# Kernel tuning notes

Measured on AMD Instinct MI355X. Metric: run time of the kernel, lower is better.

## Reference

```python
import jax, jax.numpy as jnp
import numpy as np

B, T, C, H = 8, 2048, 1024, 128

def setup_inputs() -> dict:
    key = jax.random.key(0)
    k1, k2, k3, k4 = jax.random.split(key, 4)
    s = 1.0 / np.sqrt(C)
    return {
        "x": jax.random.normal(k1, (B, T, C), dtype=jnp.float32),
        "Wq": jax.random.normal(k2, (C, H), dtype=jnp.float32) * s,
        "Wk": jax.random.normal(k3, (C, H), dtype=jnp.float32) * s,
        "Wv": jax.random.normal(k4, (C, H), dtype=jnp.float32) * s,
    }

def reference(x, Wq, Wk, Wv):
    # q,k,v: [B,T,H]
    q = jnp.einsum('btc,ch->bth', x, Wq)
    k = jnp.einsum('btc,ch->bth', x, Wk)
    v = jnp.einsum('btc,ch->bth', x, Wv)
    scale = k.shape[-1] ** -0.5
    wei = jnp.einsum('bqh,bkh->bqk', q, k) * scale  # [B,T,T]
    # NOTE: original forward never applies the tril mask -> full bidirectional softmax
    wei = jax.nn.softmax(wei, axis=-1)
    # dropout p=0 (eval): identity
    out = jnp.einsum('bqk,bkh->bqh', wei, v)  # [B,T,H]
    return out
```

## Files before the change

kernel.cpp:

```cpp
#include <hip/hip_runtime.h>

typedef __attribute__((ext_vector_type(4))) float  f32x4;
typedef __attribute__((ext_vector_type(8))) short  s16x8;
typedef __attribute__((ext_vector_type(4))) unsigned int u32x4;
typedef __attribute__((ext_vector_type(4))) unsigned short u16x4;

#define NB 8
#define NT 2048
#define NC 1024
#define NH 128
#define NM (NB * NT)

__device__ __forceinline__ unsigned short f2bf(float f) {
  union { float f; unsigned u; } v; v.f = f;
  unsigned r = v.u + 0x7FFFu + ((v.u >> 16) & 1u);
  return (unsigned short)(r >> 16);
}
__device__ __forceinline__ unsigned pack2(float a, float b) {
  return (unsigned)f2bf(a) | ((unsigned)f2bf(b) << 16);
}
__device__ __forceinline__ f32x4 mfma16(s16x8 a, s16x8 b, f32x4 c) {
  return __builtin_amdgcn_mfma_f32_16x16x32_bf16(a, b, c, 0, 0, 0);
}

__global__ __launch_bounds__(256) void k_prep_w(
    const float* __restrict__ wq, const float* __restrict__ wk,
    const float* __restrict__ wv, unsigned short* __restrict__ wt3) {
  __shared__ float ts[64][65];
  const int tid = threadIdx.x;
  const int w = blockIdx.x >> 5;
  const int rem = blockIdx.x & 31;
  const int c0 = (rem >> 1) * 64;
  const int h0 = (rem & 1) * 64;
  const float* W = (w == 0) ? wq : (w == 1) ? wk : wv;
  const int hl = tid & 63, ci = tid >> 6;
  #pragma unroll
  for (int i = 0; i < 16; ++i) {
    int cl = i * 4 + ci;
    ts[cl][hl] = W[(size_t)(c0 + cl) * NH + h0 + hl];
  }
  __syncthreads();
  const int cl2 = tid & 63, hi2 = tid >> 6;
  #pragma unroll
  for (int j = 0; j < 16; ++j) {
    int hl2 = j * 4 + hi2;
    float v = ts[cl2][hl2];
    if (w == 0) v *= 0.08838834764831845f;
    wt3[(size_t)w * 131072 + (size_t)(h0 + hl2) * NC + c0 + cl2] = f2bf(v);
  }
}

__global__ __launch_bounds__(512) void k_qkv(
    const float* __restrict__ x, const unsigned short* __restrict__ wt3,
    unsigned short* __restrict__ qo, unsigned short* __restrict__ ko,
    unsigned short* __restrict__ vo) {
  __shared__ u32x4 xs4[2 * 64 * 128 / 16];
  char* xs = (char*)xs4;
  const int tid = threadIdx.x;
  const int lane = tid & 63;
  const int w = tid >> 6;
  const int m0 = blockIdx.x * 64;

  const int sr = tid >> 3;
  const float* xp = x + (size_t)(m0 + sr) * NC + (tid & 7) * 8;
  const int wb = (sr * 128 + (tid & 7) * 16) ^ ((sr & 7) << 4);

  const int mg = w >> 2;
  const int n0 = (w & 3) * 96;
  const int arow0 = mg * 32 + (lane & 15);
  const int aswz = (arow0 & 7) << 4;
  const int akb = (lane >> 4) * 16;

  f32x4 acc[2][6] = {};
  f32x4 xa = *(const f32x4*)(xp);
  f32x4 xb = *(const f32x4*)(xp + 4);
  {
    u32x4 pk = { pack2(xa.x, xa.y), pack2(xa.z, xa.w),
                 pack2(xb.x, xb.y), pack2(xb.z, xb.w) };
    *(u32x4*)(xs + wb) = pk;
  }
  __syncthreads();

  for (int kt = 0; kt < 16; ++kt) {
    if (kt < 15) {
      xa = *(const f32x4*)(xp + (kt + 1) * 64);
      xb = *(const f32x4*)(xp + (kt + 1) * 64 + 4);
    }
    char* cb = xs + (kt & 1) * 8192;
    #pragma unroll
    for (int ks = 0; ks < 2; ++ks) {
      s16x8 a0 = *(const s16x8*)(cb + (((arow0)      * 128 + ks * 64 + akb) ^ aswz));
      s16x8 a1 = *(const s16x8*)(cb + (((arow0 + 16) * 128 + ks * 64 + akb) ^ aswz));
      const unsigned short* wp = wt3 + (size_t)(n0 + (lane & 15)) * NC
                                 + kt * 64 + ks * 32 + (lane >> 4) * 8;
      #pragma unroll
      for (int nj = 0; nj < 6; ++nj) {
        s16x8 bf = *(const s16x8*)(wp + (size_t)nj * 16 * NC);
        acc[0][nj] = mfma16(a0, bf, acc[0][nj]);
        acc[1][nj] = mfma16(a1, bf, acc[1][nj]);
      }
    }
    if (kt < 15) {
      u32x4 pk = { pack2(xa.x, xa.y), pack2(xa.z, xa.w),
                   pack2(xb.x, xb.y), pack2(xb.z, xb.w) };
      *(u32x4*)(xs + ((kt + 1) & 1) * 8192 + wb) = pk;
    }
    __syncthreads();
  }
  const int rl = (lane >> 4) * 4;
  #pragma unroll
  for (int m = 0; m < 2; ++m) {
    #pragma unroll
    for (int nj = 0; nj < 6; ++nj) {
      f32x4 a = acc[m][nj];
      int gcol = n0 + nj * 16 + (lane & 15);
      int gr = m0 + mg * 32 + m * 16 + rl;
      int h = gcol & 127;
      if (gcol < 256) {
        unsigned short* dst = (gcol < 128) ? qo : ko;
        dst[(size_t)(gr + 0) * NH + h] = f2bf(a.x);
        dst[(size_t)(gr + 1) * NH + h] = f2bf(a.y);
        dst[(size_t)(gr + 2) * NH + h] = f2bf(a.z);
        dst[(size_t)(gr + 3) * NH + h] = f2bf(a.w);
      } else {
        int bb = gr >> 11, tt = gr & 2047;
        u16x4 pv = { f2bf(a.x), f2bf(a.y), f2bf(a.z), f2bf(a.w) };
        *(u16x4*)(vo + ((size_t)(bb * NH + h) * NT + tt)) = pv;
      }
    }
  }
}

__global__ __launch_bounds__(512) void k_attn(
    const unsigned short* __restrict__ qg, const unsigned short* __restrict__ kg,
    const unsigned short* __restrict__ vg, float* __restrict__ out) {
  __shared__ u32x4 lds4[147456 / 16];
  char* L = (char*)lds4;
  const int tid = threadIdx.x;
  const int lane = tid & 63;
  const int w = tid >> 6;
  const int grp = w >> 2;
  const int wq = w & 3;
  const int gt = tid & 255;
  const int b = blockIdx.y;
  const int qr = blockIdx.x * 64 + wq * 16;
  const int c15 = lane & 15;
  const int g4 = lane >> 4;
  const int kv0 = grp * 1024;

  char* Kb0 = L + grp * 65536;
  char* Vb0 = L + grp * 65536 + 32768;
  char* pw  = L + 131072 + w * 2048;

  s16x8 qf[4];
  #pragma unroll
  for (int ks = 0; ks < 4; ++ks)
    qf[ks] = *(const s16x8*)(qg + (size_t)(b * NT + qr + c15) * NH + ks * 32 + g4 * 8);

  float m_run[4], lsum[4];
  #pragma unroll
  for (int r = 0; r < 4; ++r) { m_run[r] = -3.0e38f; lsum[r] = 0.0f; }
  f32x4 acc_o[8] = {};

  const int skr = gt >> 4;
  const unsigned short* kbase = kg + (size_t)(b * NT + kv0) * NH + (gt & 15) * 8;
  const int svh = gt >> 3;
  const unsigned short* vbase = vg + (size_t)(b * NH) * NT + kv0 + (gt & 7) * 8;

  u32x4 kreg[4], vreg[4];
  #pragma unroll
  for (int i = 0; i < 4; ++i) {
    kreg[i] = *(const u32x4*)(kbase + (size_t)(skr + i * 16) * NH);
    vreg[i] = *(const u32x4*)(vbase + (size_t)(svh + i * 32) * NT);
  }
  auto write_tiles = [&](char* Kd, char* Vd) {
    #pragma unroll
    for (int i = 0; i < 4; ++i) {
      int r = skr + i * 16;
      *(u32x4*)(Kd + ((r * 256 + (gt & 15) * 16) ^ ((r & 7) << 4))) = kreg[i];
      int h = svh + i * 32;
      *(u32x4*)(Vd + ((h * 128 + (gt & 7) * 16) ^ ((h & 7) << 4))) = vreg[i];
    }
  };
  write_tiles(Kb0, Vb0);
  __syncthreads();

  for (int kt = 0; kt < 16; ++kt) {
    char* Ks = Kb0 + (kt & 1) * 16384;
    char* Vs = Vb0 + (kt & 1) * 16384;
    if (kt < 15) {
      #pragma unroll
      for (int i = 0; i < 4; ++i) {
        kreg[i] = *(const u32x4*)(kbase + (size_t)((kt + 1) * 64 + skr + i * 16) * NH);
        vreg[i] = *(const u32x4*)(vbase + (size_t)(svh + i * 32) * NT + (kt + 1) * 64);
      }
    }
    f32x4 s[4] = {};
    __builtin_amdgcn_s_setprio(1);
    #pragma unroll
    for (int nj = 0; nj < 4; ++nj) {
      int krow = nj * 16 + c15;
      int kswz = (krow & 7) << 4;
      #pragma unroll
      for (int ks = 0; ks < 4; ++ks) {
        s16x8 bf = *(const s16x8*)(Ks + ((krow * 256 + ks * 64 + g4 * 16) ^ kswz));
        s[nj] = mfma16(qf[ks], bf, s[nj]);
      }
    }
    __builtin_amdgcn_s_setprio(0);
    float alpha[4];
    #pragma unroll
    for (int r = 0; r < 4; ++r) {
      float pm = fmaxf(fmaxf(s[0][r], s[1][r]), fmaxf(s[2][r], s[3][r]));
      pm = fmaxf(pm, __shfl_xor(pm, 1));
      pm = fmaxf(pm, __shfl_xor(pm, 2));
      pm = fmaxf(pm, __shfl_xor(pm, 4));
      pm = fmaxf(pm, __shfl_xor(pm, 8));
      float mn = fmaxf(m_run[r], pm);
      alpha[r] = __expf(m_run[r] - mn);
      m_run[r] = mn;
      float e0 = __expf(s[0][r] - mn);
      float e1 = __expf(s[1][r] - mn);
      float e2 = __expf(s[2][r] - mn);
      float e3 = __expf(s[3][r] - mn);
      s[0][r] = e0; s[1][r] = e1; s[2][r] = e2; s[3][r] = e3;
      lsum[r] = lsum[r] * alpha[r] + (e0 + e1 + e2 + e3);
    }
    #pragma unroll
    for (int hj = 0; hj < 8; ++hj) {
      acc_o[hj][0] *= alpha[0]; acc_o[hj][1] *= alpha[1];
      acc_o[hj][2] *= alpha[2]; acc_o[hj][3] *= alpha[3];
    }
    #pragma unroll
    for (int nj = 0; nj < 4; ++nj) {
      int colb = (nj * 16 + c15) * 2;
      #pragma unroll
      for (int r = 0; r < 4; ++r) {
        int row = g4 * 4 + r;
        *(unsigned short*)(pw + ((row * 128 + colb) ^ ((row & 7) << 4))) = f2bf(s[nj][r]);
      }
    }
    __builtin_amdgcn_s_setprio(1);
    #pragma unroll
    for (int ks2 = 0; ks2 < 2; ++ks2) {
      s16x8 pa = *(const s16x8*)(pw + ((c15 * 128 + ks2 * 64 + g4 * 16) ^ ((c15 & 7) << 4)));
      #pragma unroll
      for (int hj = 0; hj < 8; ++hj) {
        int vrow = hj * 16 + c15;
        s16x8 bv = *(const s16x8*)(Vs + ((vrow * 128 + ks2 * 64 + g4 * 16) ^ ((vrow & 7) << 4)));
        acc_o[hj] = mfma16(pa, bv, acc_o[hj]);
      }
    }
    __builtin_amdgcn_s_setprio(0);
    if (kt < 15) write_tiles(Kb0 + ((kt + 1) & 1) * 16384, Vb0 + ((kt + 1) & 1) * 16384);
    __syncthreads();
  }
  float l_run[4];
  #pragma unroll
  for (int r = 0; r < 4; ++r) {
    float ls = lsum[r];
    ls += __shfl_xor(ls, 1);
    ls += __shfl_xor(ls, 2);
    ls += __shfl_xor(ls, 4);
    ls += __shfl_xor(ls, 8);
    l_run[r] = ls;
  }
  float* msh = (float*)(L + 32768);
  float* lsh = (float*)(L + 32768 + 256);
  if (grp == 1) {
    #pragma unroll
    for (int r = 0; r < 4; ++r) {
      int row = wq * 16 + g4 * 4 + r;
      #pragma unroll
      for (int hj = 0; hj < 8; ++hj)
        *(float*)(L + ((row * 512 + (hj * 16 + c15) * 4) ^ ((row & 7) << 4))) = acc_o[hj][r];
      if (c15 == 0) { msh[row] = m_run[r]; lsh[row] = l_run[r]; }
    }
  }
  __syncthreads();
  if (grp == 0) {
    #pragma unroll
    for (int r = 0; r < 4; ++r) {
      int row = wq * 16 + g4 * 4 + r;
      float m1 = msh[row], l1 = lsh[row];
      float M = fmaxf(m_run[r], m1);
      float w0 = __expf(m_run[r] - M);
      float w1 = __expf(m1 - M);
      float den = 1.0f / (w0 * l_run[r] + w1 * l1);
      #pragma unroll
      for (int hj = 0; hj < 8; ++hj) {
        float o1 = *(const float*)(L + ((row * 512 + (hj * 16 + c15) * 4) ^ ((row & 7) << 4)));
        out[(size_t)(b * NT + qr + g4 * 4 + r) * NH + hj * 16 + c15] =
            (w0 * acc_o[hj][r] + w1 * o1) * den;
      }
    }
  }
}

extern "C" void kernel_launch(void* const* d_in, const int* in_sizes, int n_in,
                              void* d_out, int out_size, void* d_ws, size_t ws_size,
                              hipStream_t stream) {
  const float* x  = (const float*)d_in[0];
  const float* wq = (const float*)d_in[1];
  const float* wk = (const float*)d_in[2];
  const float* wv = (const float*)d_in[3];
  unsigned short* ws  = (unsigned short*)d_ws;
  unsigned short* qb  = ws;
  unsigned short* kb  = ws + (size_t)2 * 1024 * 1024;
  unsigned short* vb  = ws + (size_t)4 * 1024 * 1024;
  unsigned short* wt3 = ws + (size_t)6 * 1024 * 1024;

  k_prep_w<<<dim3(96), dim3(256), 0, stream>>>(wq, wk, wv, wt3);
  k_qkv<<<dim3(NM / 64), dim3(512), 0, stream>>>(x, wt3, qb, kb, vb);
  k_attn<<<dim3(NT / 64, NB), dim3(512), 0, stream>>>(qb, kb, vb, (float*)d_out);
}
```

Measured before the change: 189.3 us.

## Shrink tiles and split attention KV across four wave groups for occupancy

The QKV projection now uses 32-row blocks with each wave covering 48 output columns, which doubles the grid and shrinks LDS. The attention kernel now splits KV four ways, with 512 keys per group. It processes 32 query rows per block using 32-key tiles held in a single LDS buffer, so LDS drops from about 144KB to about 73KB. Four partial softmax states are merged at the end. The aim is more resident blocks per CU and better latency hiding, but the loss of double buffering adds an extra barrier per iteration, and the MFMA work per sync is smaller.

```diff
diff --git a/kernel.cpp b/kernel.cpp
--- a/kernel.cpp
+++ b/kernel.cpp
@@ -3,6 +3,7 @@
 typedef __attribute__((ext_vector_type(4))) float  f32x4;
 typedef __attribute__((ext_vector_type(8))) short  s16x8;
 typedef __attribute__((ext_vector_type(4))) unsigned int u32x4;
+typedef __attribute__((ext_vector_type(2))) unsigned int u32x2;
 typedef __attribute__((ext_vector_type(4))) unsigned short u16x4;
 
 #define NB 8
@@ -50,71 +51,65 @@
   }
 }
 
-__global__ __launch_bounds__(512) void k_qkv(
+__global__ __launch_bounds__(512, 4) void k_qkv(
     const float* __restrict__ x, const unsigned short* __restrict__ wt3,
     unsigned short* __restrict__ qo, unsigned short* __restrict__ ko,
     unsigned short* __restrict__ vo) {
-  __shared__ u32x4 xs4[2 * 64 * 128 / 16];
+  __shared__ u32x4 xs4[8192 / 16];
   char* xs = (char*)xs4;
   const int tid = threadIdx.x;
   const int lane = tid & 63;
   const int w = tid >> 6;
-  const int m0 = blockIdx.x * 64;
-
-  const int sr = tid >> 3;
-  const float* xp = x + (size_t)(m0 + sr) * NC + (tid & 7) * 8;
-  const int wb = (sr * 128 + (tid & 7) * 16) ^ ((sr & 7) << 4);
-
-  const int mg = w >> 2;
-  const int n0 = (w & 3) * 96;
-  const int arow0 = mg * 32 + (lane & 15);
-  const int aswz = (arow0 & 7) << 4;
-  const int akb = (lane >> 4) * 16;
-
-  f32x4 acc[2][6] = {};
-  f32x4 xa = *(const f32x4*)(xp);
-  f32x4 xb = *(const f32x4*)(xp + 4);
+  const int m0 = blockIdx.x * 32;
+  const int c15 = lane & 15;
+  const int g4 = lane >> 4;
+
+  const int sr = tid >> 4;
+  const float* xp = x + (size_t)(m0 + sr) * NC + (tid & 15) * 4;
+  const int wb = (sr * 128 + (tid & 15) * 8) ^ ((sr & 7) << 4);
+
+  const int n0 = w * 48;
+  const int aswz = (c15 & 7) << 4;
+  const int akb = g4 * 16;
+
+  f32x4 acc[2][3] = {};
+  f32x4 xr = *(const f32x4*)(xp);
   {
-    u32x4 pk = { pack2(xa.x, xa.y), pack2(xa.z, xa.w),
-                 pack2(xb.x, xb.y), pack2(xb.z, xb.w) };
-    *(u32x4*)(xs + wb) = pk;
+    u32x2 pk = { pack2(xr.x, xr.y), pack2(xr.z, xr.w) };
+    *(u32x2*)(xs + wb) = pk;
   }
   __syncthreads();
 
   for (int kt = 0; kt < 16; ++kt) {
-    if (kt < 15) {
-      xa = *(const f32x4*)(xp + (kt + 1) * 64);
-      xb = *(const f32x4*)(xp + (kt + 1) * 64 + 4);
-    }
-    char* cb = xs + (kt & 1) * 8192;
+    if (kt < 15) xr = *(const f32x4*)(xp + (kt + 1) * 64);
+    char* cb = xs + (kt & 1) * 4096;
     #pragma unroll
     for (int ks = 0; ks < 2; ++ks) {
-      s16x8 a0 = *(const s16x8*)(cb + (((arow0)      * 128 + ks * 64 + akb) ^ aswz));
-      s16x8 a1 = *(const s16x8*)(cb + (((arow0 + 16) * 128 + ks * 64 + akb) ^ aswz));
-      const unsigned short* wp = wt3 + (size_t)(n0 + (lane & 15)) * NC
-                                 + kt * 64 + ks * 32 + (lane >> 4) * 8;
-      #pragma unroll
-      for (int nj = 0; nj < 6; ++nj) {
+      s16x8 a0 = *(const s16x8*)(cb + (((c15)      * 128 + ks * 64 + akb) ^ aswz));
+      s16x8 a1 = *(const s16x8*)(cb + (((c15 + 16) * 128 + ks * 64 + akb) ^ aswz));
+      const unsigned short* wp = wt3 + (size_t)(n0 + c15) * NC
+                                 + kt * 64 + ks * 32 + g4 * 8;
+      #pragma unroll
+      for (int nj = 0; nj < 3; ++nj) {
         s16x8 bf = *(const s16x8*)(wp + (size_t)nj * 16 * NC);
         acc[0][nj] = mfma16(a0, bf, acc[0][nj]);
         acc[1][nj] = mfma16(a1, bf, acc[1][nj]);
       }
     }
     if (kt < 15) {
-      u32x4 pk = { pack2(xa.x, xa.y), pack2(xa.z, xa.w),
-                   pack2(xb.x, xb.y), pack2(xb.z, xb.w) };
-      *(u32x4*)(xs + ((kt + 1) & 1) * 8192 + wb) = pk;
+      u32x2 pk = { pack2(xr.x, xr.y), pack2(xr.z, xr.w) };
+      *(u32x2*)(xs + ((kt + 1) & 1) * 4096 + wb) = pk;
     }
     __syncthreads();
   }
-  const int rl = (lane >> 4) * 4;
+  const int rl = g4 * 4;
   #pragma unroll
   for (int m = 0; m < 2; ++m) {
     #pragma unroll
-    for (int nj = 0; nj < 6; ++nj) {
+    for (int nj = 0; nj < 3; ++nj) {
       f32x4 a = acc[m][nj];
-      int gcol = n0 + nj * 16 + (lane & 15);
-      int gr = m0 + mg * 32 + m * 16 + rl;
+      int gcol = n0 + nj * 16 + c15;
+      int gr = m0 + m * 16 + rl;
       int h = gcol & 127;
       if (gcol < 256) {
         unsigned short* dst = (gcol < 128) ? qo : ko;
@@ -131,79 +126,79 @@
   }
 }
 
-__global__ __launch_bounds__(512) void k_attn(
+__global__ __launch_bounds__(512, 4) void k_attn(
     const unsigned short* __restrict__ qg, const unsigned short* __restrict__ kg,
     const unsigned short* __restrict__ vg, float* __restrict__ out) {
-  __shared__ u32x4 lds4[147456 / 16];
+  __shared__ u32x4 lds4[74752 / 16];
   char* L = (char*)lds4;
   const int tid = threadIdx.x;
   const int lane = tid & 63;
   const int w = tid >> 6;
-  const int grp = w >> 2;
-  const int wq = w & 3;
-  const int gt = tid & 255;
+  const int grp = w & 3;
+  const int qs = w >> 2;
+  const int gl = qs * 64 + lane;
   const int b = blockIdx.y;
-  const int qr = blockIdx.x * 64 + wq * 16;
+  const int qr0 = blockIdx.x * 32;
   const int c15 = lane & 15;
   const int g4 = lane >> 4;
-  const int kv0 = grp * 1024;
-
-  char* Kb0 = L + grp * 65536;
-  char* Vb0 = L + grp * 65536 + 32768;
-  char* pw  = L + 131072 + w * 2048;
+  const int kv0 = grp * 512;
+
+  char* Kg = L + grp * 16384;
+  char* Vg = Kg + 8192;
+  char* pw = L + 65536 + w * 1024;
+  float* msh = (float*)(L + 73728);
+  float* lsh = msh + 96;
 
   s16x8 qf[4];
   #pragma unroll
   for (int ks = 0; ks < 4; ++ks)
-    qf[ks] = *(const s16x8*)(qg + (size_t)(b * NT + qr + c15) * NH + ks * 32 + g4 * 8);
+    qf[ks] = *(const s16x8*)(qg + (size_t)(b * NT + qr0 + qs * 16 + c15) * NH + ks * 32 + g4 * 8);
 
   float m_run[4], lsum[4];
   #pragma unroll
   for (int r = 0; r < 4; ++r) { m_run[r] = -3.0e38f; lsum[r] = 0.0f; }
   f32x4 acc_o[8] = {};
 
-  const int skr = gt >> 4;
-  const unsigned short* kbase = kg + (size_t)(b * NT + kv0) * NH + (gt & 15) * 8;
-  const int svh = gt >> 3;
-  const unsigned short* vbase = vg + (size_t)(b * NH) * NT + kv0 + (gt & 7) * 8;
+  const int krow = gl >> 4;
+  const unsigned short* kptr = kg + (size_t)(b * NT + kv0 + krow) * NH + (gl & 15) * 8;
+  const int vh = gl >> 2;
+  const unsigned short* vptr = vg + (size_t)(b * NH + vh) * NT + kv0 + (gl & 3) * 8;
 
   u32x4 kreg[4], vreg[4];
   #pragma unroll
   for (int i = 0; i < 4; ++i) {
-    kreg[i] = *(const u32x4*)(kbase + (size_t)(skr + i * 16) * NH);
-    vreg[i] = *(const u32x4*)(vbase + (size_t)(svh + i * 32) * NT);
-  }
-  auto write_tiles = [&](char* Kd, char* Vd) {
+    kreg[i] = *(const u32x4*)(kptr + (size_t)(i * 8) * NH);
+    vreg[i] = *(const u32x4*)(vptr + (size_t)(i * 32) * NT);
+  }
+  auto write_tiles = [&]() {
     #pragma unroll
     for (int i = 0; i < 4; ++i) {
-      int r = skr + i * 16;
-      *(u32x4*)(Kd + ((r * 256 + (gt & 15) * 16) ^ ((r & 7) << 4))) = kreg[i];
-      int h = svh + i * 32;
-      *(u32x4*)(Vd + ((h * 128 + (gt & 7) * 16) ^ ((h & 7) << 4))) = vreg[i];
+      int r = krow + i * 8;
+      *(u32x4*)(Kg + ((r * 256 + (gl & 15) * 16) ^ ((r & 7) << 4))) = kreg[i];
+      int h = vh + i * 32;
+      int rr = h >> 1;
+      *(u32x4*)(Vg + ((rr * 128 + (h & 1) * 64 + (gl & 3) * 16) ^ ((rr & 7) << 4))) = vreg[i];
     }
   };
-  write_tiles(Kb0, Vb0);
+  write_tiles();
   __syncthreads();
 
   for (int kt = 0; kt < 16; ++kt) {
-    char* Ks = Kb0 + (kt & 1) * 16384;
-    char* Vs = Vb0 + (kt & 1) * 16384;
     if (kt < 15) {
       #pragma unroll
       for (int i = 0; i < 4; ++i) {
-        kreg[i] = *(const u32x4*)(kbase + (size_t)((kt + 1) * 64 + skr + i * 16) * NH);
-        vreg[i] = *(const u32x4*)(vbase + (size_t)(svh + i * 32) * NT + (kt + 1) * 64);
-      }
-    }
-    f32x4 s[4] = {};
+        kreg[i] = *(const u32x4*)(kptr + (size_t)((kt + 1) * 32 + i * 8) * NH);
+        vreg[i] = *(const u32x4*)(vptr + (size_t)(i * 32) * NT + (kt + 1) * 32);
+      }
+    }
+    f32x4 s[2] = {};
     __builtin_amdgcn_s_setprio(1);
     #pragma unroll
-    for (int nj = 0; nj < 4; ++nj) {
-      int krow = nj * 16 + c15;
-      int kswz = (krow & 7) << 4;
+    for (int nj = 0; nj < 2; ++nj) {
+      int kr = nj * 16 + c15;
       #pragma unroll
       for (int ks = 0; ks < 4; ++ks) {
-        s16x8 bf = *(const s16x8*)(Ks + ((krow * 256 + ks * 64 + g4 * 16) ^ kswz));
+        s16x8 bf = *(const s16x8*)(Kg + ((kr * 256 + ks * 64 + g4 * 16) ^ ((kr & 7) << 4)));
         s[nj] = mfma16(qf[ks], bf, s[nj]);
       }
     }
@@ -211,7 +206,7 @@
     float alpha[4];
     #pragma unroll
     for (int r = 0; r < 4; ++r) {
-      float pm = fmaxf(fmaxf(s[0][r], s[1][r]), fmaxf(s[2][r], s[3][r]));
+      float pm = fmaxf(s[0][r], s[1][r]);
       pm = fmaxf(pm, __shfl_xor(pm, 1));
       pm = fmaxf(pm, __shfl_xor(pm, 2));
       pm = fmaxf(pm, __shfl_xor(pm, 4));
@@ -221,10 +216,8 @@
       m_run[r] = mn;
       float e0 = __expf(s[0][r] - mn);
       float e1 = __expf(s[1][r] - mn);
-      float e2 = __expf(s[2][r] - mn);
-      float e3 = __expf(s[3][r] - mn);
-      s[0][r] = e0; s[1][r] = e1; s[2][r] = e2; s[3][r] = e3;
-      lsum[r] = lsum[r] * alpha[r] + (e0 + e1 + e2 + e3);
+      s[0][r] = e0; s[1][r] = e1;
+      lsum[r] = lsum[r] * alpha[r] + (e0 + e1);
     }
     #pragma unroll
     for (int hj = 0; hj < 8; ++hj) {
@@ -232,27 +225,29 @@
       acc_o[hj][2] *= alpha[2]; acc_o[hj][3] *= alpha[3];
     }
     #pragma unroll
-    for (int nj = 0; nj < 4; ++nj) {
-      int colb = (nj * 16 + c15) * 2;
+    for (int nj = 0; nj < 2; ++nj) {
       #pragma unroll
       for (int r = 0; r < 4; ++r) {
         int row = g4 * 4 + r;
-        *(unsigned short*)(pw + ((row * 128 + colb) ^ ((row & 7) << 4))) = f2bf(s[nj][r]);
+        int pr = row >> 1;
+        *(unsigned short*)(pw + ((pr * 128 + (row & 1) * 64 + (nj * 16 + c15) * 2)
+                                 ^ ((pr & 7) << 4))) = f2bf(s[nj][r]);
       }
     }
     __builtin_amdgcn_s_setprio(1);
-    #pragma unroll
-    for (int ks2 = 0; ks2 < 2; ++ks2) {
-      s16x8 pa = *(const s16x8*)(pw + ((c15 * 128 + ks2 * 64 + g4 * 16) ^ ((c15 & 7) << 4)));
+    {
+      int ppr = c15 >> 1;
+      s16x8 pa = *(const s16x8*)(pw + ((ppr * 128 + (c15 & 1) * 64 + g4 * 16) ^ ((ppr & 7) << 4)));
       #pragma unroll
       for (int hj = 0; hj < 8; ++hj) {
-        int vrow = hj * 16 + c15;
-        s16x8 bv = *(const s16x8*)(Vs + ((vrow * 128 + ks2 * 64 + g4 * 16) ^ ((vrow & 7) << 4)));
+        int rr = hj * 8 + (c15 >> 1);
+        s16x8 bv = *(const s16x8*)(Vg + ((rr * 128 + (c15 & 1) * 64 + g4 * 16) ^ ((rr & 7) << 4)));
         acc_o[hj] = mfma16(pa, bv, acc_o[hj]);
       }
     }
     __builtin_amdgcn_s_setprio(0);
-    if (kt < 15) write_tiles(Kb0 + ((kt + 1) & 1) * 16384, Vb0 + ((kt + 1) & 1) * 16384);
+    __syncthreads();
+    if (kt < 15) write_tiles();
     __syncthreads();
   }
   float l_run[4];
@@ -265,33 +260,46 @@
     ls += __shfl_xor(ls, 8);
     l_run[r] = ls;
   }
-  float* msh = (float*)(L + 32768);
-  float* lsh = (float*)(L + 32768 + 256);
-  if (grp == 1) {
+  if (grp > 0) {
+    char* mb = L + (grp - 1) * 16384;
     #pragma unroll
     for (int r = 0; r < 4; ++r) {
-      int row = wq * 16 + g4 * 4 + r;
+      int row = qs * 16 + g4 * 4 + r;
       #pragma unroll
       for (int hj = 0; hj < 8; ++hj)
-        *(float*)(L + ((row * 512 + (hj * 16 + c15) * 4) ^ ((row & 7) << 4))) = acc_o[hj][r];
-      if (c15 == 0) { msh[row] = m_run[r]; lsh[row] = l_run[r]; }
+        *(float*)(mb + row * 512 + (hj * 16 + c15) * 4) = acc_o[hj][r];
+      if (c15 == 0) {
+        msh[(grp - 1) * 32 + row] = m_run[r];
+        lsh[(grp - 1) * 32 + row] = l_run[r];
+      }
     }
   }
   __syncthreads();
   if (grp == 0) {
     #pragma unroll
     for (int r = 0; r < 4; ++r) {
-      int row = wq * 16 + g4 * 4 + r;
-      float m1 = msh[row], l1 = lsh[row];
-      float M = fmaxf(m_run[r], m1);
+      int row = qs * 16 + g4 * 4 + r;
+      float M = m_run[r];
+      float mg[3], lg[3];
+      #pragma unroll
+      for (int g = 0; g < 3; ++g) {
+        mg[g] = msh[g * 32 + row];
+        lg[g] = lsh[g * 32 + row];
+        M = fmaxf(M, mg[g]);
+      }
       float w0 = __expf(m_run[r] - M);
-      float w1 = __expf(m1 - M);
-      float den = 1.0f / (w0 * l_run[r] + w1 * l1);
+      float wg[3];
+      float den = w0 * l_run[r];
+      #pragma unroll
+      for (int g = 0; g < 3; ++g) { wg[g] = __expf(mg[g] - M); den += wg[g] * lg[g]; }
+      float inv = 1.0f / den;
       #pragma unroll
       for (int hj = 0; hj < 8; ++hj) {
-        float o1 = *(const float*)(L + ((row * 512 + (hj * 16 + c15) * 4) ^ ((row & 7) << 4)));
-        out[(size_t)(b * NT + qr + g4 * 4 + r) * NH + hj * 16 + c15] =
-            (w0 * acc_o[hj][r] + w1 * o1) * den;
+        float o = w0 * acc_o[hj][r];
+        #pragma unroll
+        for (int g = 0; g < 3; ++g)
+          o += wg[g] * *(const float*)(L + g * 16384 + row * 512 + (hj * 16 + c15) * 4);
+        out[(size_t)(b * NT + qr0 + row) * NH + hj * 16 + c15] = o * inv;
       }
     }
   }
@@ -311,6 +319,6 @@
   unsigned short* wt3 = ws + (size_t)6 * 1024 * 1024;
 
   k_prep_w<<<dim3(96), dim3(256), 0, stream>>>(wq, wk, wv, wt3);
-  k_qkv<<<dim3(NM / 64), dim3(512), 0, stream>>>(x, wt3, qb, kb, vb);
-  k_attn<<<dim3(NT / 64, NB), dim3(512), 0, stream>>>(qb, kb, vb, (float*)d_out);
-}
+  k_qkv<<<dim3(NM / 32), dim3(512), 0, stream>>>(x, wt3, qb, kb, vb);
+  k_attn<<<dim3(NT / 32, NB), dim3(512), 0, stream>>>(qb, kb, vb, (float*)d_out);
+}
```

Result: slower. 245.1 us (+29.5%).

## Restructure QKV projection blocks and attention KV tiles to 128-wide single-buffered stages

Applied to the files above, without the earlier changes.

The QKV projection kernel now uses 256-thread blocks covering 32 rows with a K step of 128, which doubles the number of blocks and allows three blocks per CU. The attention kernel interleaves the two KV-split groups across waves and moves from double-buffered 64-key tiles to single-buffered 128-key tiles held in registers. This halves the loop iterations but adds an extra barrier around each LDS tile write. The P·V step is split into two halves so the 64-column per-wave P scratch can be reused. Register pressure rises (8 K and 8 V staging registers, 8 score accumulators), which risks spills under the occupancy hint of two blocks per CU.

```diff
diff --git a/kernel.cpp b/kernel.cpp
--- a/kernel.cpp
+++ b/kernel.cpp
@@ -50,49 +50,53 @@
   }
 }
 
-__global__ __launch_bounds__(512) void k_qkv(
+__global__ __launch_bounds__(256, 3) void k_qkv(
     const float* __restrict__ x, const unsigned short* __restrict__ wt3,
     unsigned short* __restrict__ qo, unsigned short* __restrict__ ko,
     unsigned short* __restrict__ vo) {
-  __shared__ u32x4 xs4[2 * 64 * 128 / 16];
+  __shared__ u32x4 xs4[16384 / 16];
   char* xs = (char*)xs4;
   const int tid = threadIdx.x;
   const int lane = tid & 63;
   const int w = tid >> 6;
-  const int m0 = blockIdx.x * 64;
+  const int m0 = blockIdx.x * 32;
+  const int c15 = lane & 15;
+  const int g4 = lane >> 4;
 
   const int sr = tid >> 3;
-  const float* xp = x + (size_t)(m0 + sr) * NC + (tid & 7) * 8;
-  const int wb = (sr * 128 + (tid & 7) * 16) ^ ((sr & 7) << 4);
-
-  const int mg = w >> 2;
-  const int n0 = (w & 3) * 96;
-  const int arow0 = mg * 32 + (lane & 15);
-  const int aswz = (arow0 & 7) << 4;
-  const int akb = (lane >> 4) * 16;
+  const float* xp = x + (size_t)(m0 + sr) * NC + (tid & 7) * 16;
+  const int wb = (sr * 256 + (tid & 7) * 32) ^ ((sr & 7) << 4);
+
+  const int n0 = w * 96;
+  const int aswz = (c15 & 7) << 4;
 
   f32x4 acc[2][6] = {};
-  f32x4 xa = *(const f32x4*)(xp);
-  f32x4 xb = *(const f32x4*)(xp + 4);
-  {
-    u32x4 pk = { pack2(xa.x, xa.y), pack2(xa.z, xa.w),
-                 pack2(xb.x, xb.y), pack2(xb.z, xb.w) };
-    *(u32x4*)(xs + wb) = pk;
-  }
+  f32x4 xr[4];
+  #pragma unroll
+  for (int j = 0; j < 4; ++j) xr[j] = *(const f32x4*)(xp + j * 4);
+  auto pack_write = [&](int buf) {
+    u32x4 gA = { pack2(xr[0].x, xr[0].y), pack2(xr[0].z, xr[0].w),
+                 pack2(xr[1].x, xr[1].y), pack2(xr[1].z, xr[1].w) };
+    u32x4 gB = { pack2(xr[2].x, xr[2].y), pack2(xr[2].z, xr[2].w),
+                 pack2(xr[3].x, xr[3].y), pack2(xr[3].z, xr[3].w) };
+    *(u32x4*)(xs + buf * 8192 + wb) = gA;
+    *(u32x4*)(xs + buf * 8192 + ((sr * 256 + (tid & 7) * 32 + 16) ^ ((sr & 7) << 4))) = gB;
+  };
+  pack_write(0);
   __syncthreads();
 
-  for (int kt = 0; kt < 16; ++kt) {
-    if (kt < 15) {
-      xa = *(const f32x4*)(xp + (kt + 1) * 64);
-      xb = *(const f32x4*)(xp + (kt + 1) * 64 + 4);
+  for (int kt = 0; kt < 8; ++kt) {
+    if (kt < 7) {
+      #pragma unroll
+      for (int j = 0; j < 4; ++j) xr[j] = *(const f32x4*)(xp + (kt + 1) * 128 + j * 4);
     }
     char* cb = xs + (kt & 1) * 8192;
     #pragma unroll
-    for (int ks = 0; ks < 2; ++ks) {
-      s16x8 a0 = *(const s16x8*)(cb + (((arow0)      * 128 + ks * 64 + akb) ^ aswz));
-      s16x8 a1 = *(const s16x8*)(cb + (((arow0 + 16) * 128 + ks * 64 + akb) ^ aswz));
-      const unsigned short* wp = wt3 + (size_t)(n0 + (lane & 15)) * NC
-                                 + kt * 64 + ks * 32 + (lane >> 4) * 8;
+    for (int ks = 0; ks < 4; ++ks) {
+      s16x8 a0 = *(const s16x8*)(cb + (((c15)      * 256 + ks * 64 + g4 * 16) ^ aswz));
+      s16x8 a1 = *(const s16x8*)(cb + (((c15 + 16) * 256 + ks * 64 + g4 * 16) ^ aswz));
+      const unsigned short* wp = wt3 + (size_t)(n0 + c15) * NC
+                                 + kt * 128 + ks * 32 + g4 * 8;
       #pragma unroll
       for (int nj = 0; nj < 6; ++nj) {
         s16x8 bf = *(const s16x8*)(wp + (size_t)nj * 16 * NC);
@@ -100,21 +104,17 @@
         acc[1][nj] = mfma16(a1, bf, acc[1][nj]);
       }
     }
-    if (kt < 15) {
-      u32x4 pk = { pack2(xa.x, xa.y), pack2(xa.z, xa.w),
-                   pack2(xb.x, xb.y), pack2(xb.z, xb.w) };
-      *(u32x4*)(xs + ((kt + 1) & 1) * 8192 + wb) = pk;
-    }
+    if (kt < 7) pack_write((kt + 1) & 1);
     __syncthreads();
   }
-  const int rl = (lane >> 4) * 4;
+  const int rl = g4 * 4;
   #pragma unroll
   for (int m = 0; m < 2; ++m) {
     #pragma unroll
     for (int nj = 0; nj < 6; ++nj) {
       f32x4 a = acc[m][nj];
-      int gcol = n0 + nj * 16 + (lane & 15);
-      int gr = m0 + mg * 32 + m * 16 + rl;
+      int gcol = n0 + nj * 16 + c15;
+      int gr = m0 + m * 16 + rl;
       int h = gcol & 127;
       if (gcol < 256) {
         unsigned short* dst = (gcol < 128) ? qo : ko;
@@ -131,7 +131,7 @@
   }
 }
 
-__global__ __launch_bounds__(512) void k_attn(
+__global__ __launch_bounds__(512, 2) void k_attn(
     const unsigned short* __restrict__ qg, const unsigned short* __restrict__ kg,
     const unsigned short* __restrict__ vg, float* __restrict__ out) {
   __shared__ u32x4 lds4[147456 / 16];
@@ -139,79 +139,76 @@
   const int tid = threadIdx.x;
   const int lane = tid & 63;
   const int w = tid >> 6;
-  const int grp = w >> 2;
-  const int wq = w & 3;
-  const int gt = tid & 255;
+  const int grp = w & 1;
+  const int qs = w >> 1;
+  const int gl = qs * 64 + lane;
   const int b = blockIdx.y;
-  const int qr = blockIdx.x * 64 + wq * 16;
+  const int qr0 = blockIdx.x * 64;
   const int c15 = lane & 15;
   const int g4 = lane >> 4;
   const int kv0 = grp * 1024;
 
-  char* Kb0 = L + grp * 65536;
-  char* Vb0 = L + grp * 65536 + 32768;
-  char* pw  = L + 131072 + w * 2048;
+  char* Kg = L + grp * 65536;
+  char* Vg = Kg + 32768;
+  char* pw = L + 131072 + w * 2048;
 
   s16x8 qf[4];
   #pragma unroll
   for (int ks = 0; ks < 4; ++ks)
-    qf[ks] = *(const s16x8*)(qg + (size_t)(b * NT + qr + c15) * NH + ks * 32 + g4 * 8);
+    qf[ks] = *(const s16x8*)(qg + (size_t)(b * NT + qr0 + qs * 16 + c15) * NH + ks * 32 + g4 * 8);
 
   float m_run[4], lsum[4];
   #pragma unroll
   for (int r = 0; r < 4; ++r) { m_run[r] = -3.0e38f; lsum[r] = 0.0f; }
   f32x4 acc_o[8] = {};
 
-  const int skr = gt >> 4;
-  const unsigned short* kbase = kg + (size_t)(b * NT + kv0) * NH + (gt & 15) * 8;
-  const int svh = gt >> 3;
-  const unsigned short* vbase = vg + (size_t)(b * NH) * NT + kv0 + (gt & 7) * 8;
-
-  u32x4 kreg[4], vreg[4];
-  #pragma unroll
-  for (int i = 0; i < 4; ++i) {
-    kreg[i] = *(const u32x4*)(kbase + (size_t)(skr + i * 16) * NH);
-    vreg[i] = *(const u32x4*)(vbase + (size_t)(svh + i * 32) * NT);
-  }
-  auto write_tiles = [&](char* Kd, char* Vd) {
-    #pragma unroll
-    for (int i = 0; i < 4; ++i) {
-      int r = skr + i * 16;
-      *(u32x4*)(Kd + ((r * 256 + (gt & 15) * 16) ^ ((r & 7) << 4))) = kreg[i];
-      int h = svh + i * 32;
-      *(u32x4*)(Vd + ((h * 128 + (gt & 7) * 16) ^ ((h & 7) << 4))) = vreg[i];
+  const int srow = gl >> 4;
+  const unsigned short* kptr = kg + (size_t)(b * NT + kv0 + srow) * NH + (gl & 15) * 8;
+  const unsigned short* vptr = vg + (size_t)(b * NH + srow) * NT + kv0 + (gl & 15) * 8;
+
+  u32x4 kreg[8], vreg[8];
+  auto stage = [&](int kt) {
+    #pragma unroll
+    for (int i = 0; i < 8; ++i) {
+      kreg[i] = *(const u32x4*)(kptr + ((size_t)(kt * 128 + i * 16)) * NH);
+      vreg[i] = *(const u32x4*)(vptr + (size_t)(i * 16) * NT + kt * 128);
     }
   };
-  write_tiles(Kb0, Vb0);
+  auto write_tiles = [&]() {
+    #pragma unroll
+    for (int i = 0; i < 8; ++i) {
+      int r = srow + i * 16;
+      int off = (r * 256 + (gl & 15) * 16) ^ ((r & 7) << 4);
+      *(u32x4*)(Kg + off) = kreg[i];
+      *(u32x4*)(Vg + off) = vreg[i];
+    }
+  };
+  stage(0);
+  write_tiles();
   __syncthreads();
 
-  for (int kt = 0; kt < 16; ++kt) {
-    char* Ks = Kb0 + (kt & 1) * 16384;
-    char* Vs = Vb0 + (kt & 1) * 16384;
-    if (kt < 15) {
-      #pragma unroll
-      for (int i = 0; i < 4; ++i) {
-        kreg[i] = *(const u32x4*)(kbase + (size_t)((kt + 1) * 64 + skr + i * 16) * NH);
-        vreg[i] = *(const u32x4*)(vbase + (size_t)(svh + i * 32) * NT + (kt + 1) * 64);
-      }
-    }
-    f32x4 s[4] = {};
+  for (int kt = 0; kt < 8; ++kt) {
+    if (kt < 7) stage(kt + 1);
+    f32x4 s[8];
     __builtin_amdgcn_s_setprio(1);
     #pragma unroll
-    for (int nj = 0; nj < 4; ++nj) {
-      int krow = nj * 16 + c15;
-      int kswz = (krow & 7) << 4;
+    for (int nj = 0; nj < 8; ++nj) {
+      f32x4 acc_s = {};
+      int kr = nj * 16 + c15;
+      int kswz = (kr & 7) << 4;
       #pragma unroll
       for (int ks = 0; ks < 4; ++ks) {
-        s16x8 bf = *(const s16x8*)(Ks + ((krow * 256 + ks * 64 + g4 * 16) ^ kswz));
-        s[nj] = mfma16(qf[ks], bf, s[nj]);
-      }
+        s16x8 bf = *(const s16x8*)(Kg + ((kr * 256 + ks * 64 + g4 * 16) ^ kswz));
+        acc_s = mfma16(qf[ks], bf, acc_s);
+      }
+      s[nj] = acc_s;
     }
     __builtin_amdgcn_s_setprio(0);
     float alpha[4];
     #pragma unroll
     for (int r = 0; r < 4; ++r) {
-      float pm = fmaxf(fmaxf(s[0][r], s[1][r]), fmaxf(s[2][r], s[3][r]));
+      float pm = fmaxf(fmaxf(fmaxf(s[0][r], s[1][r]), fmaxf(s[2][r], s[3][r])),
+                       fmaxf(fmaxf(s[4][r], s[5][r]), fmaxf(s[6][r], s[7][r])));
       pm = fmaxf(pm, __shfl_xor(pm, 1));
       pm = fmaxf(pm, __shfl_xor(pm, 2));
       pm = fmaxf(pm, __shfl_xor(pm, 4));
@@ -219,12 +216,14 @@
       float mn = fmaxf(m_run[r], pm);
       alpha[r] = __expf(m_run[r] - mn);
       m_run[r] = mn;
-      float e0 = __expf(s[0][r] - mn);
-      float e1 = __expf(s[1][r] - mn);
-      float e2 = __expf(s[2][r] - mn);
-      float e3 = __expf(s[3][r] - mn);
-      s[0][r] = e0; s[1][r] = e1; s[2][r] = e2; s[3][r] = e3;
-      lsum[r] = lsum[r] * alpha[r] + (e0 + e1 + e2 + e3);
+      float psum = 0.0f;
+      #pragma unroll
+      for (int nj = 0; nj < 8; ++nj) {
+        float e = __expf(s[nj][r] - mn);
+        s[nj][r] = e;
+        psum += e;
+      }
+      lsum[r] = lsum[r] * alpha[r] + psum;
     }
     #pragma unroll
     for (int hj = 0; hj < 8; ++hj) {
@@ -232,27 +231,32 @@
       acc_o[hj][2] *= alpha[2]; acc_o[hj][3] *= alpha[3];
     }
     #pragma unroll
-    for (int nj = 0; nj < 4; ++nj) {
-      int colb = (nj * 16 + c15) * 2;
-      #pragma unroll
-      for (int r = 0; r < 4; ++r) {
-        int row = g4 * 4 + r;
-        *(unsigned short*)(pw + ((row * 128 + colb) ^ ((row & 7) << 4))) = f2bf(s[nj][r]);
-      }
-    }
-    __builtin_amdgcn_s_setprio(1);
-    #pragma unroll
-    for (int ks2 = 0; ks2 < 2; ++ks2) {
-      s16x8 pa = *(const s16x8*)(pw + ((c15 * 128 + ks2 * 64 + g4 * 16) ^ ((c15 & 7) << 4)));
-      #pragma unroll
-      for (int hj = 0; hj < 8; ++hj) {
-        int vrow = hj * 16 + c15;
-        s16x8 bv = *(const s16x8*)(Vs + ((vrow * 128 + ks2 * 64 + g4 * 16) ^ ((vrow & 7) << 4)));
-        acc_o[hj] = mfma16(pa, bv, acc_o[hj]);
-      }
-    }
-    __builtin_amdgcn_s_setprio(0);
-    if (kt < 15) write_tiles(Kb0 + ((kt + 1) & 1) * 16384, Vb0 + ((kt + 1) & 1) * 16384);
+    for (int half = 0; half < 2; ++half) {
+      #pragma unroll
+      for (int nj = 0; nj < 4; ++nj) {
+        #pragma unroll
+        for (int r = 0; r < 4; ++r) {
+          int row = g4 * 4 + r;
+          *(unsigned short*)(pw + ((row * 128 + (nj * 16 + c15) * 2) ^ ((row & 7) << 4)))
+              = f2bf(s[half * 4 + nj][r]);
+        }
+      }
+      __builtin_amdgcn_s_setprio(1);
+      #pragma unroll
+      for (int ks2 = 0; ks2 < 2; ++ks2) {
+        s16x8 pa = *(const s16x8*)(pw + ((c15 * 128 + ks2 * 64 + g4 * 16) ^ ((c15 & 7) << 4)));
+        int vcb = (half * 2 + ks2) * 64 + g4 * 16;
+        #pragma unroll
+        for (int hj = 0; hj < 8; ++hj) {
+          int vr = hj * 16 + c15;
+          s16x8 bv = *(const s16x8*)(Vg + ((vr * 256 + vcb) ^ ((vr & 7) << 4)));
+          acc_o[hj] = mfma16(pa, bv, acc_o[hj]);
+        }
+      }
+      __builtin_amdgcn_s_setprio(0);
+    }
+    __syncthreads();
+    if (kt < 7) write_tiles();
     __syncthreads();
   }
   float l_run[4];
@@ -265,15 +269,15 @@
     ls += __shfl_xor(ls, 8);
     l_run[r] = ls;
   }
-  float* msh = (float*)(L + 32768);
-  float* lsh = (float*)(L + 32768 + 256);
+  float* msh = (float*)(L + 131072);
+  float* lsh = msh + 64;
   if (grp == 1) {
     #pragma unroll
     for (int r = 0; r < 4; ++r) {
-      int row = wq * 16 + g4 * 4 + r;
+      int row = qs * 16 + g4 * 4 + r;
       #pragma unroll
       for (int hj = 0; hj < 8; ++hj)
-        *(float*)(L + ((row * 512 + (hj * 16 + c15) * 4) ^ ((row & 7) << 4))) = acc_o[hj][r];
+        *(float*)(L + row * 512 + (hj * 16 + c15) * 4) = acc_o[hj][r];
       if (c15 == 0) { msh[row] = m_run[r]; lsh[row] = l_run[r]; }
     }
   }
@@ -281,7 +285,7 @@
   if (grp == 0) {
     #pragma unroll
     for (int r = 0; r < 4; ++r) {
-      int row = wq * 16 + g4 * 4 + r;
+      int row = qs * 16 + g4 * 4 + r;
       float m1 = msh[row], l1 = lsh[row];
       float M = fmaxf(m_run[r], m1);
       float w0 = __expf(m_run[r] - M);
@@ -289,8 +293,8 @@
       float den = 1.0f / (w0 * l_run[r] + w1 * l1);
       #pragma unroll
       for (int hj = 0; hj < 8; ++hj) {
-        float o1 = *(const float*)(L + ((row * 512 + (hj * 16 + c15) * 4) ^ ((row & 7) << 4)));
-        out[(size_t)(b * NT + qr + g4 * 4 + r) * NH + hj * 16 + c15] =
+        float o1 = *(const float*)(L + row * 512 + (hj * 16 + c15) * 4);
+        out[(size_t)(b * NT + qr0 + row) * NH + hj * 16 + c15] =
             (w0 * acc_o[hj][r] + w1 * o1) * den;
       }
     }
@@ -311,6 +315,6 @@
   unsigned short* wt3 = ws + (size_t)6 * 1024 * 1024;
 
   k_prep_w<<<dim3(96), dim3(256), 0, stream>>>(wq, wk, wv, wt3);
-  k_qkv<<<dim3(NM / 64), dim3(512), 0, stream>>>(x, wt3, qb, kb, vb);
+  k_qkv<<<dim3(NM / 32), dim3(256), 0, stream>>>(x, wt3, qb, kb, vb);
   k_attn<<<dim3(NT / 64, NB), dim3(512), 0, stream>>>(qb, kb, vb, (float*)d_out);
 }
```

Result: no change. 191.6 us (+1.2%).
